# Performance work log

Measured on AMD Instinct MI355X. Metric: run time of the kernel, lower is better.

The kernel has to match this reference:

```python
import math
import jax, jax.numpy as jnp
import numpy as np

D_MODEL = 512
NUM_HEADS = 8
FACTOR = 128
B, T = 16, 768


def setup_inputs() -> dict:
    key = jax.random.key(0)
    ks = jax.random.split(key, 8)
    s_in = 1.0 / math.sqrt(D_MODEL)
    x = jax.random.normal(ks[0], (B, T, D_MODEL), dtype=jnp.float32)
    Wqkv = jax.random.normal(ks[1], (3 * D_MODEL, D_MODEL), dtype=jnp.float32) * s_in
    bqkv = jax.random.normal(ks[2], (3 * D_MODEL,), dtype=jnp.float32) * s_in
    Wconv = jax.random.normal(ks[3], (D_MODEL, D_MODEL, 3), dtype=jnp.float32) * (1.0 / math.sqrt(3 * D_MODEL))
    bconv = jax.random.normal(ks[4], (D_MODEL,), dtype=jnp.float32) * s_in
    gamma = jnp.ones((D_MODEL,), dtype=jnp.float32)
    beta = jnp.zeros((D_MODEL,), dtype=jnp.float32)
    return {"x": x, "Wqkv": Wqkv, "bqkv": bqkv, "Wconv": Wconv, "bconv": bconv, "gamma": gamma, "beta": beta}


def reference(x, Wqkv, bqkv, Wconv, bconv, gamma, beta):
    Bq, Tq, D = x.shape
    H, dk = NUM_HEADS, D // NUM_HEADS
    # --- ProbAttention ---
    qkv = x @ Wqkv.T + bqkv                         # [B,T,3D]
    q, k, v = jnp.split(qkv, 3, axis=-1)
    q = q.reshape(Bq, Tq, H, dk).transpose(0, 2, 1, 3)   # [B,H,T,dk]
    k = k.reshape(Bq, Tq, H, dk).transpose(0, 2, 1, 3)
    v = v.reshape(Bq, Tq, H, dk).transpose(0, 2, 1, 3)
    U = FACTOR * int(math.log(Tq))                  # == T for our config
    scores = jnp.einsum('bhqd,bhkd->bhqk', q, k) / math.sqrt(dk)  # [B,H,T,T]
    top_vals, _ = jax.lax.top_k(scores, U)          # descending-sorted, like torch.topk
    attn = jax.nn.softmax(top_vals, axis=-1)        # [B,H,T,U]
    out = jnp.einsum('bhqu,bhud->bhqd', attn, v)    # requires U == T, as in torch
    attn_out = out.transpose(0, 2, 1, 3).reshape(Bq, Tq, D)
    # --- strided conv branch: Conv1d(D, D, k=3, s=2, p=1) ---
    xc = x.transpose(0, 2, 1)                       # [B,D,T]
    yc = jax.lax.conv_general_dilated(xc, Wconv, window_strides=(2,), padding=[(1, 1)],
                                      dimension_numbers=('NCH', 'OIH', 'NCH'))
    yc = yc + bconv[None, :, None]
    x_conv = yc.transpose(0, 2, 1)                  # [B,T//2,D]
    # --- residual + LayerNorm ---
    res = attn_out[:, ::2, :] + x_conv
    mu = jnp.mean(res, axis=-1, keepdims=True)
    var = jnp.mean(jnp.square(res - mu), axis=-1, keepdims=True)
    y = (res - mu) * jax.lax.rsqrt(var + 1e-5) * gamma + beta
    return y  # dropout is identity in eval mode
```

## Files before the change

kernel.cpp:

```cpp
#include <hip/hip_runtime.h>
#include <hip/hip_bf16.h>
#include <hip/hip_fp16.h>
#include <stdint.h>
#include <math.h>

#define TSEQ 768
#define TOUT 384
#define DM   512
#define NH   8
#define DKH  64

typedef short bf16x8 __attribute__((ext_vector_type(8)));
typedef float f32x4  __attribute__((ext_vector_type(4)));
typedef __fp16 f16x2 __attribute__((ext_vector_type(2)));

__device__ __forceinline__ unsigned short f2bf(float f){
  unsigned int u = __float_as_uint(f);
  unsigned int r = (u + 0x7FFFu + ((u >> 16) & 1u)) >> 16;
  return (unsigned short)r;
}

#define MFMA(a,b,c) __builtin_amdgcn_mfma_f32_16x16x32_bf16((a),(b),(c),0,0,0)

typedef __attribute__((address_space(1))) const void* gas_ptr;
typedef __attribute__((address_space(3))) void*       las_ptr;
__device__ __forceinline__ void gload16(const void* g, void* l){
  __builtin_amdgcn_global_load_lds((gas_ptr)g, (las_ptr)l, 16, 0, 0);
}

__device__ __forceinline__ unsigned xlane_xor_u(unsigned x, int dl){
  int xi = (int)x;
  if (dl == 1)      return (unsigned)__builtin_amdgcn_update_dpp(xi, xi, 0xB1, 0xF, 0xF, true);
  else if (dl == 2) return (unsigned)__builtin_amdgcn_update_dpp(xi, xi, 0x4E, 0xF, 0xF, true);
  else if (dl == 4) return (unsigned)__builtin_amdgcn_ds_swizzle(xi, 0x101F);
  else if (dl == 8) return (unsigned)__builtin_amdgcn_update_dpp(xi, xi, 0x128, 0xF, 0xF, true);
  else return (unsigned)__shfl_xor(xi, dl, 64);
}
__device__ __forceinline__ float xlane_xor_f(float x, int dl){
  return __int_as_float((int)xlane_xor_u((unsigned)__float_as_int(x), dl));
}

__device__ __forceinline__ unsigned pmax2(unsigned a, unsigned b){
  f16x2 r = __builtin_elementwise_max(*reinterpret_cast<f16x2*>(&a),
                                      *reinterpret_cast<f16x2*>(&b));
  return *reinterpret_cast<unsigned*>(&r);
}
__device__ __forceinline__ unsigned pmin2(unsigned a, unsigned b){
  f16x2 r = __builtin_elementwise_min(*reinterpret_cast<f16x2*>(&a),
                                      *reinterpret_cast<f16x2*>(&b));
  return *reinterpret_cast<unsigned*>(&r);
}
__device__ __forceinline__ unsigned pkrtz(float a, float b){
  f16x2 h = __builtin_amdgcn_cvt_pkrtz(a, b);
  return *reinterpret_cast<unsigned*>(&h);
}
__device__ __forceinline__ float lo16f(unsigned u){
  f16x2 h = *reinterpret_cast<f16x2*>(&u); return (float)h[0];
}
__device__ __forceinline__ float hi16f(unsigned u){
  f16x2 h = *reinterpret_cast<f16x2*>(&u); return (float)h[1];
}

__global__ __launch_bounds__(256) void k_cvt(const float* __restrict__ in,
                                             unsigned short* __restrict__ out, int n){
  int i = (blockIdx.x * 256 + threadIdx.x) * 8;
  if (i >= n) return;
  float4 a = *reinterpret_cast<const float4*>(in + i);
  float4 b = *reinterpret_cast<const float4*>(in + i + 4);
  unsigned short u[8] = {f2bf(a.x),f2bf(a.y),f2bf(a.z),f2bf(a.w),
                         f2bf(b.x),f2bf(b.y),f2bf(b.z),f2bf(b.w)};
  *reinterpret_cast<bf16x8*>(out + i) = *reinterpret_cast<bf16x8*>(u);
}

__global__ __launch_bounds__(256) void k_cvt_wconv(const float* __restrict__ w,
                                                   unsigned short* __restrict__ o){
  int idx = blockIdx.x * 256 + threadIdx.x;
  float w0 = w[idx*3+0], w1 = w[idx*3+1], w2 = w[idx*3+2];
  o[idx]          = f2bf(w0);
  o[262144 + idx] = f2bf(w1);
  o[524288 + idx] = f2bf(w2);
}

__global__ __launch_bounds__(256) void k_qkv(const unsigned short* __restrict__ xb,
    const unsigned short* __restrict__ wq, const float* __restrict__ bias,
    unsigned short* __restrict__ qe, unsigned short* __restrict__ kb,
    unsigned short* __restrict__ vb){
  __shared__ unsigned short sA[128*32];
  __shared__ unsigned short sB[128*32];
  int bm = blockIdx.x % 96, bn = blockIdx.x / 96;
  int m0 = bm*128, n0 = bn*128;
  int tid = threadIdx.x, w = tid>>6, l = tid&63;
  int wr = w>>1, wc = w&1, lr = l&15, lk = (l>>4)*8;

  int srow = w*32 + (l>>2);
  int scol = (l&3)*8;
  const unsigned short* gA = xb + (size_t)(m0 + srow)*DM + scol;
  const unsigned short* gB = wq + (size_t)(n0 + srow)*DM + scol;
  unsigned short* dA = sA + w*1024;
  unsigned short* dB = sB + w*1024;

  const unsigned short* ra = sA + (wr*64 + lr)*32 + lk;
  const unsigned short* rb = sB + (wc*64 + lr)*32 + lk;

  f32x4 z = {0.f,0.f,0.f,0.f};
  f32x4 acc[4][4] = {{z,z,z,z},{z,z,z,z},{z,z,z,z},{z,z,z,z}};

  #pragma unroll 1
  for (int ks=0; ks<16; ++ks){
    int k0 = ks*32;
    gload16(gA + k0,          dA);
    gload16(gA + 16*DM + k0,  dA + 512);
    gload16(gB + k0,          dB);
    gload16(gB + 16*DM + k0,  dB + 512);
    __syncthreads();
    bf16x8 af[4], bfr[4];
    #pragma unroll
    for (int f=0; f<4; ++f){
      af[f]  = *reinterpret_cast<const bf16x8*>(ra + f*512);
      bfr[f] = *reinterpret_cast<const bf16x8*>(rb + f*512);
    }
    #pragma unroll
    for (int fq=0; fq<4; ++fq)
      #pragma unroll
      for (int fn=0; fn<4; ++fn)
        acc[fq][fn] = MFMA(af[fq], bfr[fn], acc[fq][fn]);
    __syncthreads();
  }

  int region = n0 >> 9;
  #pragma unroll
  for (int fq=0; fq<4; ++fq)
    #pragma unroll
    for (int fn=0; fn<4; ++fn)
      #pragma unroll
      for (int r=0; r<4; ++r){
        int m = m0 + wr*64 + fq*16 + (l>>4)*4 + r;
        int b = m / TSEQ, t = m - b*TSEQ;
        int n = n0 + wc*64 + fn*16 + lr;
        float val = acc[fq][fn][r] + bias[n];
        unsigned short bv = f2bf(val);
        int bh = b*NH + ((n>>6)&7); int d = n & 63;
        if (region == 0){ if((t&1)==0) qe[((size_t)bh*TOUT + (t>>1))*DKH + d] = bv; }
        else if (region == 1){ kb[((size_t)bh*TSEQ + t)*DKH + d] = bv; }
        else { vb[((size_t)bh*TSEQ + t)*DKH + d] = bv; }
      }
}

__global__ __launch_bounds__(256) void k_vt(const unsigned short* __restrict__ vb,
                                            unsigned short* __restrict__ vT){
  __shared__ unsigned short tile[64][72];
  int bh = blockIdx.x / 12, tt = blockIdx.x % 12;
  int t0 = tt*64;
  int tid = threadIdx.x;
  int r = tid >> 2, c0 = (tid & 3) * 16;
  const unsigned short* src = vb + ((size_t)bh*TSEQ + t0 + r)*DKH + c0;
  *reinterpret_cast<bf16x8*>(&tile[r][c0])   = *reinterpret_cast<const bf16x8*>(src);
  *reinterpret_cast<bf16x8*>(&tile[r][c0+8]) = *reinterpret_cast<const bf16x8*>(src + 8);
  __syncthreads();
  int d = r;
  unsigned short tmp[16];
  #pragma unroll
  for (int j=0;j<16;++j) tmp[j] = tile[c0+j][d];
  unsigned short* dst = vT + ((size_t)bh*DKH + d)*TSEQ + t0 + c0;
  *reinterpret_cast<bf16x8*>(dst)     = *reinterpret_cast<bf16x8*>(tmp);
  *reinterpret_cast<bf16x8*>(dst + 8) = *reinterpret_cast<bf16x8*>(tmp + 8);
}

#define SQ_ROWB 3088
__global__ __launch_bounds__(512, 4) void k_attn(const unsigned short* __restrict__ qe,
    const unsigned short* __restrict__ kb, const unsigned short* __restrict__ vT,
    float* __restrict__ attn){
  __shared__ alignas(16) char sq_raw[16*SQ_ROWB];
  int bh = blockIdx.x / 24, qb = blockIdx.x % 24;
  int tid = threadIdx.x, w = tid>>6, l = tid&63, lr = l&15, lk = (l>>4)*8;

  const unsigned short* qbase = qe + ((size_t)bh*TOUT + qb*16)*DKH;
  bf16x8 qa0 = *reinterpret_cast<const bf16x8*>(qbase + lr*DKH + lk);
  bf16x8 qa1 = *reinterpret_cast<const bf16x8*>(qbase + lr*DKH + 32 + lk);
  const unsigned short* kbase = kb + (size_t)bh*TSEQ*DKH;
  #pragma unroll
  for (int i=0;i<6;++i){
    int nt = w + 8*i;
    const unsigned short* kr = kbase + (size_t)(nt*16 + lr)*DKH + lk;
    bf16x8 B0 = *reinterpret_cast<const bf16x8*>(kr);
    bf16x8 B1 = *reinterpret_cast<const bf16x8*>(kr + 32);
    f32x4 c = {0.f,0.f,0.f,0.f};
    c = MFMA(qa0,B0,c);
    c = MFMA(qa1,B1,c);
    int col = nt*16 + lr;
    int A = col*4;
    int sw = A ^ (((A >> 8) & 7) << 4);
    #pragma unroll
    for (int r=0;r<4;++r){
      int qr = (l>>4)*4 + r;
      *reinterpret_cast<float*>(sq_raw + qr*SQ_ROWB + sw) = c[r] * 0.125f;
    }
  }
  __syncthreads();

  {
    char* rowA = sq_raw + (w*2)*SQ_ROWB;
    char* rowB = rowA + SQ_ROWB;
    unsigned wv[16];
    if (l < 48){
      #pragma unroll
      for (int i4=0;i4<4;++i4){
        int A = l*64 + i4*16;
        int Asw = A ^ (((A >> 8) & 7) << 4);
        f32x4 va = *reinterpret_cast<f32x4*>(rowA + Asw);
        f32x4 vb = *reinterpret_cast<f32x4*>(rowB + Asw);
        wv[i4*4+0] = pkrtz(va[0], vb[0]);
        wv[i4*4+1] = pkrtz(va[1], vb[1]);
        wv[i4*4+2] = pkrtz(va[2], vb[2]);
        wv[i4*4+3] = pkrtz(va[3], vb[3]);
      }
    } else {
      #pragma unroll
      for (int j=0;j<16;++j) wv[j] = 0xFC00FC00u;
    }
    int lane16 = l << 4;
    #pragma unroll
    for (int k = 2; k <= 1024; k <<= 1){
      #pragma unroll
      for (int D = k>>1; D >= 16; D >>= 1){
        int dl = D >> 4;
        bool sel = ((lane16 & k) == 0) == ((l & dl) == 0);
        #pragma unroll
        for (int j=0;j<16;++j){
          unsigned y  = xlane_xor_u(wv[j], dl);
          unsigned mx = pmax2(wv[j], y), mn = pmin2(wv[j], y);
          wv[j] = sel ? mx : mn;
        }
      }
      #pragma unroll
      for (int D = ((k>>1) > 8 ? 8 : (k>>1)); D >= 1; D >>= 1){
        #pragma unroll
        for (int j=0;j<16;++j){
          if ((j & D) == 0){
            int j2 = j | D;
            unsigned mx = pmax2(wv[j], wv[j2]), mn = pmin2(wv[j], wv[j2]);
            if (k <= 8){
              if ((j & k) == 0){ wv[j] = mx; wv[j2] = mn; }
              else             { wv[j] = mn; wv[j2] = mx; }
            } else {
              bool up = (k == 16) ? ((l & 1) == 0) : ((lane16 & k) == 0);
              wv[j]  = up ? mx : mn;
              wv[j2] = up ? mn : mx;
            }
          }
        }
      }
    }
    #pragma unroll 1
    for (int half=0; half<2; ++half){
      float xf[16];
      #pragma unroll
      for (int j=0;j<16;++j) xf[j] = half ? hi16f(wv[j]) : lo16f(wv[j]);
      float mx0 = __shfl(xf[0], 0, 64);
      float s = 0.f;
      #pragma unroll
      for (int j=0;j<16;++j){ xf[j] = __expf(xf[j]-mx0); s += xf[j]; }
      #pragma unroll
      for (int o=1;o<64;o<<=1) s += xlane_xor_f(s, o);
      float inv = 1.f / s;
      if (l < 48){
        unsigned short u[16];
        #pragma unroll
        for (int j=0;j<16;++j) u[j] = f2bf(xf[j]*inv);
        char* pp = (half ? rowB : rowA) + l*32;
        *reinterpret_cast<bf16x8*>(pp)      = *reinterpret_cast<bf16x8*>(u);
        *reinterpret_cast<bf16x8*>(pp + 16) = *reinterpret_cast<bf16x8*>(u + 8);
      }
    }
  }
  __syncthreads();

  if (w < 4){
    f32x4 o = {0.f,0.f,0.f,0.f};
    const unsigned short* vtb = vT + ((size_t)bh*DKH + w*16 + lr)*TSEQ + lk;
    const char* prow = sq_raw + lr*SQ_ROWB + (l>>4)*16;
    #pragma unroll
    for (int ks=0; ks<24; ++ks){
      bf16x8 a  = *reinterpret_cast<const bf16x8*>(prow + ks*64);
      bf16x8 bb = *reinterpret_cast<const bf16x8*>(vtb + ks*32);
      o = MFMA(a,bb,o);
    }
    int b = bh >> 3, h = bh & 7;
    float* ab = attn + ((size_t)b*TOUT + qb*16)*DM + h*DKH + w*16 + lr;
    #pragma unroll
    for (int r=0;r<4;++r){
      int qr = (l>>4)*4 + r;
      ab[(size_t)qr*DM] = o[r];
    }
  }
}

__global__ __launch_bounds__(256) void k_conv(const unsigned short* __restrict__ xb,
    const unsigned short* __restrict__ wc, const float* __restrict__ bconv,
    float* __restrict__ res){
  __shared__ unsigned short sA[128*32];
  __shared__ unsigned short sB[128*32];
  int bm = blockIdx.x % 48, bn = blockIdx.x / 48;
  int m0 = bm*128, n0 = bn*128;
  int tid = threadIdx.x, w = tid>>6, l = tid&63;
  int wr = w>>1, wc2 = w&1, lr = l&15, lk = (l>>4)*8;
  int b = m0 / TOUT, t0 = m0 - b*TOUT;

  int srow = w*32 + (l>>2);
  int scol = (l&3)*8;
  const unsigned short* xrow = xb + (size_t)b*TSEQ*DM;
  unsigned short* dA = sA + w*1024;
  unsigned short* dB = sB + w*1024;
  const unsigned short* ra  = sA + (wr*64 + lr)*32 + lk;
  const unsigned short* rb_ = sB + (wc2*64 + lr)*32 + lk;

  f32x4 z = {0.f,0.f,0.f,0.f};
  f32x4 acc[4][4] = {{z,z,z,z},{z,z,z,z},{z,z,z,z},{z,z,z,z}};
  bool zfix = (t0 == 0);

  #pragma unroll 1
  for (int j=0; j<3; ++j){
    int tin0 = 2*(t0 + srow) + j - 1;
    int tin0c = tin0 < 0 ? 0 : tin0;
    const unsigned short* gA0 = xrow + (size_t)tin0c*DM + scol;
    const unsigned short* gA1 = xrow + (size_t)(tin0 + 32)*DM + scol;
    const unsigned short* gB  = wc + (size_t)j*262144 + (size_t)(n0 + srow)*DM + scol;
    bool dz = zfix && (j == 0);
    #pragma unroll 1
    for (int ks=0; ks<16; ++ks){
      int k0 = ks*32;
      gload16(gA0 + k0,         dA);
      gload16(gA1 + k0,         dA + 512);
      gload16(gB + k0,          dB);
      gload16(gB + 16*DM + k0,  dB + 512);
      __syncthreads();
      if (dz && tid < 4){
        bf16x8 zz = {0,0,0,0,0,0,0,0};
        *reinterpret_cast<bf16x8*>(sA + tid*8) = zz;
      }
      __syncthreads();
      bf16x8 af[4], bfr[4];
      #pragma unroll
      for (int f=0; f<4; ++f){
        af[f]  = *reinterpret_cast<const bf16x8*>(ra  + f*512);
        bfr[f] = *reinterpret_cast<const bf16x8*>(rb_ + f*512);
      }
      #pragma unroll
      for (int fq=0; fq<4; ++fq)
        #pragma unroll
        for (int fn=0; fn<4; ++fn)
          acc[fq][fn] = MFMA(af[fq], bfr[fn], acc[fq][fn]);
      __syncthreads();
    }
  }

  #pragma unroll
  for (int fq=0; fq<4; ++fq)
    #pragma unroll
    for (int fn=0; fn<4; ++fn)
      #pragma unroll
      for (int r=0; r<4; ++r){
        int t = t0 + wr*64 + fq*16 + (l>>4)*4 + r;
        int n = n0 + wc2*64 + fn*16 + lr;
        size_t idx = ((size_t)b*TOUT + t)*DM + n;
        res[idx] = acc[fq][fn][r] + bconv[n] + res[idx];
      }
}

__global__ __launch_bounds__(256) void k_ln(const float* __restrict__ res,
    const float* __restrict__ gamma, const float* __restrict__ beta,
    float* __restrict__ out){
  int row = blockIdx.x*4 + (threadIdx.x>>6);
  int l = threadIdx.x & 63;
  const float* rp = res + (size_t)row*DM + l*8;
  float4 v0 = *reinterpret_cast<const float4*>(rp);
  float4 v1 = *reinterpret_cast<const float4*>(rp + 4);
  float s = v0.x+v0.y+v0.z+v0.w + v1.x+v1.y+v1.z+v1.w;
  #pragma unroll
  for (int o=1;o<64;o<<=1) s += __shfl_xor(s, o, 64);
  float mean = s * (1.f/512.f);
  float d0=v0.x-mean, d1=v0.y-mean, d2=v0.z-mean, d3=v0.w-mean;
  float d4=v1.x-mean, d5=v1.y-mean, d6=v1.z-mean, d7=v1.w-mean;
  float q = d0*d0+d1*d1+d2*d2+d3*d3+d4*d4+d5*d5+d6*d6+d7*d7;
  #pragma unroll
  for (int o=1;o<64;o<<=1) q += __shfl_xor(q, o, 64);
  float var = q * (1.f/512.f);
  float inv = rsqrtf(var + 1e-5f);
  float4 g0 = *reinterpret_cast<const float4*>(gamma + l*8);
  float4 g1 = *reinterpret_cast<const float4*>(gamma + l*8 + 4);
  float4 b0 = *reinterpret_cast<const float4*>(beta + l*8);
  float4 b1 = *reinterpret_cast<const float4*>(beta + l*8 + 4);
  float4 o0, o1;
  o0.x = d0*inv*g0.x + b0.x; o0.y = d1*inv*g0.y + b0.y;
  o0.z = d2*inv*g0.z + b0.z; o0.w = d3*inv*g0.w + b0.w;
  o1.x = d4*inv*g1.x + b1.x; o1.y = d5*inv*g1.y + b1.y;
  o1.z = d6*inv*g1.z + b1.z; o1.w = d7*inv*g1.w + b1.w;
  float* op = out + (size_t)row*DM + l*8;
  *reinterpret_cast<float4*>(op)     = o0;
  *reinterpret_cast<float4*>(op + 4) = o1;
}

extern "C" void kernel_launch(void* const* d_in, const int* in_sizes, int n_in,
                              void* d_out, int out_size, void* d_ws, size_t ws_size,
                              hipStream_t stream){
  const float* x     = (const float*)d_in[0];
  const float* Wqkv  = (const float*)d_in[1];
  const float* bqkv  = (const float*)d_in[2];
  const float* Wconv = (const float*)d_in[3];
  const float* bconv = (const float*)d_in[4];
  const float* gamma = (const float*)d_in[5];
  const float* beta  = (const float*)d_in[6];
  float* out = (float*)d_out;

  char* ws = (char*)d_ws;
  size_t off = 0;
  auto alloc = [&](size_t bytes)->char*{
    char* p = ws + off; off += (bytes + 255) & ~(size_t)255; return p;
  };
  unsigned short* xb  = (unsigned short*)alloc(6291456ull*2);
  unsigned short* wqb = (unsigned short*)alloc(786432ull*2);
  unsigned short* wc3 = (unsigned short*)alloc(786432ull*2);
  unsigned short* qeb = (unsigned short*)alloc(3145728ull*2);
  unsigned short* kbb = (unsigned short*)alloc(6291456ull*2);
  unsigned short* vbb = (unsigned short*)alloc(6291456ull*2);
  unsigned short* vtb = (unsigned short*)alloc(6291456ull*2);
  float*          resb = (float*)alloc(3145728ull*4);

  k_cvt<<<dim3(3072), dim3(256), 0, stream>>>(x, xb, 6291456);
  k_cvt<<<dim3(384),  dim3(256), 0, stream>>>(Wqkv, wqb, 786432);
  k_cvt_wconv<<<dim3(1024), dim3(256), 0, stream>>>(Wconv, wc3);
  k_qkv<<<dim3(1152), dim3(256), 0, stream>>>(xb, wqb, bqkv, qeb, kbb, vbb);
  k_vt<<<dim3(1536), dim3(256), 0, stream>>>(vbb, vtb);
  k_attn<<<dim3(3072), dim3(512), 0, stream>>>(qeb, kbb, vtb, resb);
  k_conv<<<dim3(192), dim3(256), 0, stream>>>(xb, wc3, bconv, resb);
  k_ln<<<dim3(1536), dim3(256), 0, stream>>>(resb, gamma, beta, out);
}
```

Measured before the change: 240.7 us.

## Merge conversion kernels, simplify bitonic sort direction, halve conv N-tile

The three fp32-to-bf16 conversion launches become one kernel that dispatches on block index, removing two launches. The bitonic sort in the attention kernel now flips the sign bit of the packed fp16 values so that every stage sorts in a single direction, which drops the per-lane direction selects. The conv GEMM tile narrows from 128 to 64 output columns, doubling the grid from 192 to 384 blocks to fill more CUs, at the cost of reading more A tiles per output.

```diff
diff --git a/kernel.cpp b/kernel.cpp
--- a/kernel.cpp
+++ b/kernel.cpp
@@ -61,24 +61,33 @@
   f16x2 h = *reinterpret_cast<f16x2*>(&u); return (float)h[1];
 }
 
-__global__ __launch_bounds__(256) void k_cvt(const float* __restrict__ in,
-                                             unsigned short* __restrict__ out, int n){
-  int i = (blockIdx.x * 256 + threadIdx.x) * 8;
-  if (i >= n) return;
-  float4 a = *reinterpret_cast<const float4*>(in + i);
-  float4 b = *reinterpret_cast<const float4*>(in + i + 4);
+__device__ __forceinline__ void cvt8(const float* __restrict__ in,
+                                     unsigned short* __restrict__ out){
+  float4 a = *reinterpret_cast<const float4*>(in);
+  float4 b = *reinterpret_cast<const float4*>(in + 4);
   unsigned short u[8] = {f2bf(a.x),f2bf(a.y),f2bf(a.z),f2bf(a.w),
                          f2bf(b.x),f2bf(b.y),f2bf(b.z),f2bf(b.w)};
-  *reinterpret_cast<bf16x8*>(out + i) = *reinterpret_cast<bf16x8*>(u);
-}
-
-__global__ __launch_bounds__(256) void k_cvt_wconv(const float* __restrict__ w,
-                                                   unsigned short* __restrict__ o){
-  int idx = blockIdx.x * 256 + threadIdx.x;
-  float w0 = w[idx*3+0], w1 = w[idx*3+1], w2 = w[idx*3+2];
-  o[idx]          = f2bf(w0);
-  o[262144 + idx] = f2bf(w1);
-  o[524288 + idx] = f2bf(w2);
+  *reinterpret_cast<bf16x8*>(out) = *reinterpret_cast<bf16x8*>(u);
+}
+
+__global__ __launch_bounds__(256) void k_cvt_all(const float* __restrict__ x,
+    const float* __restrict__ wq, const float* __restrict__ wconv,
+    unsigned short* __restrict__ xb, unsigned short* __restrict__ wqb,
+    unsigned short* __restrict__ wc3){
+  int bid = blockIdx.x;
+  if (bid < 3072){
+    int i = (bid*256 + threadIdx.x)*8;
+    cvt8(x + i, xb + i);
+  } else if (bid < 3456){
+    int i = ((bid-3072)*256 + threadIdx.x)*8;
+    cvt8(wq + i, wqb + i);
+  } else {
+    int idx = (bid-3456)*256 + threadIdx.x;
+    float w0 = wconv[idx*3+0], w1 = wconv[idx*3+1], w2 = wconv[idx*3+2];
+    wc3[idx]          = f2bf(w0);
+    wc3[262144 + idx] = f2bf(w1);
+    wc3[524288 + idx] = f2bf(w2);
+  }
 }
 
 __global__ __launch_bounds__(256) void k_qkv(const unsigned short* __restrict__ xb,
@@ -218,34 +227,47 @@
       #pragma unroll
       for (int j=0;j<16;++j) wv[j] = 0xFC00FC00u;
     }
-    int lane16 = l << 4;
     #pragma unroll
     for (int k = 2; k <= 1024; k <<= 1){
-      #pragma unroll
-      for (int D = k>>1; D >= 16; D >>= 1){
-        int dl = D >> 4;
-        bool sel = ((lane16 & k) == 0) == ((l & dl) == 0);
-        #pragma unroll
-        for (int j=0;j<16;++j){
-          unsigned y  = xlane_xor_u(wv[j], dl);
-          unsigned mx = pmax2(wv[j], y), mn = pmin2(wv[j], y);
-          wv[j] = sel ? mx : mn;
+      if (k >= 16){
+        bool up = (k == 16) ? ((l & 1) == 0) : ((l & (k >> 4)) == 0);
+        unsigned negmask = up ? 0u : 0x80008000u;
+        #pragma unroll
+        for (int j=0;j<16;++j) wv[j] ^= negmask;
+        #pragma unroll
+        for (int D = k>>1; D >= 16; D >>= 1){
+          int dl = D >> 4;
+          bool sel = (l & dl) == 0;
+          #pragma unroll
+          for (int j=0;j<16;++j){
+            unsigned y  = xlane_xor_u(wv[j], dl);
+            unsigned mx = pmax2(wv[j], y), mn = pmin2(wv[j], y);
+            wv[j] = sel ? mx : mn;
+          }
         }
-      }
-      #pragma unroll
-      for (int D = ((k>>1) > 8 ? 8 : (k>>1)); D >= 1; D >>= 1){
-        #pragma unroll
-        for (int j=0;j<16;++j){
-          if ((j & D) == 0){
-            int j2 = j | D;
-            unsigned mx = pmax2(wv[j], wv[j2]), mn = pmin2(wv[j], wv[j2]);
-            if (k <= 8){
+        #pragma unroll
+        for (int D = 8; D >= 1; D >>= 1){
+          #pragma unroll
+          for (int j=0;j<16;++j){
+            if ((j & D) == 0){
+              int j2 = j | D;
+              unsigned mx = pmax2(wv[j], wv[j2]), mn = pmin2(wv[j], wv[j2]);
+              wv[j] = mx; wv[j2] = mn;
+            }
+          }
+        }
+        #pragma unroll
+        for (int j=0;j<16;++j) wv[j] ^= negmask;
+      } else {
+        #pragma unroll
+        for (int D = k>>1; D >= 1; D >>= 1){
+          #pragma unroll
+          for (int j=0;j<16;++j){
+            if ((j & D) == 0){
+              int j2 = j | D;
+              unsigned mx = pmax2(wv[j], wv[j2]), mn = pmin2(wv[j], wv[j2]);
               if ((j & k) == 0){ wv[j] = mx; wv[j2] = mn; }
               else             { wv[j] = mn; wv[j2] = mx; }
-            } else {
-              bool up = (k == 16) ? ((l & 1) == 0) : ((lane16 & k) == 0);
-              wv[j]  = up ? mx : mn;
-              wv[j2] = up ? mn : mx;
             }
           }
         }
@@ -299,56 +321,55 @@
     const unsigned short* __restrict__ wc, const float* __restrict__ bconv,
     float* __restrict__ res){
   __shared__ unsigned short sA[128*32];
-  __shared__ unsigned short sB[128*32];
+  __shared__ unsigned short sB[64*32];
   int bm = blockIdx.x % 48, bn = blockIdx.x / 48;
-  int m0 = bm*128, n0 = bn*128;
+  int m0 = bm*128, n0 = bn*64;
   int tid = threadIdx.x, w = tid>>6, l = tid&63;
   int wr = w>>1, wc2 = w&1, lr = l&15, lk = (l>>4)*8;
   int b = m0 / TOUT, t0 = m0 - b*TOUT;
 
-  int srow = w*32 + (l>>2);
+  int srowA = w*32 + (l>>2);
+  int srowB = w*16 + (l>>2);
   int scol = (l&3)*8;
   const unsigned short* xrow = xb + (size_t)b*TSEQ*DM;
   unsigned short* dA = sA + w*1024;
-  unsigned short* dB = sB + w*1024;
+  unsigned short* dB = sB + w*512;
   const unsigned short* ra  = sA + (wr*64 + lr)*32 + lk;
-  const unsigned short* rb_ = sB + (wc2*64 + lr)*32 + lk;
+  const unsigned short* rb_ = sB + (wc2*32 + lr)*32 + lk;
 
   f32x4 z = {0.f,0.f,0.f,0.f};
-  f32x4 acc[4][4] = {{z,z,z,z},{z,z,z,z},{z,z,z,z},{z,z,z,z}};
+  f32x4 acc[4][2] = {{z,z},{z,z},{z,z},{z,z}};
   bool zfix = (t0 == 0);
 
   #pragma unroll 1
   for (int j=0; j<3; ++j){
-    int tin0 = 2*(t0 + srow) + j - 1;
+    int tin0 = 2*(t0 + srowA) + j - 1;
     int tin0c = tin0 < 0 ? 0 : tin0;
     const unsigned short* gA0 = xrow + (size_t)tin0c*DM + scol;
     const unsigned short* gA1 = xrow + (size_t)(tin0 + 32)*DM + scol;
-    const unsigned short* gB  = wc + (size_t)j*262144 + (size_t)(n0 + srow)*DM + scol;
+    const unsigned short* gB  = wc + (size_t)j*262144 + (size_t)(n0 + srowB)*DM + scol;
     bool dz = zfix && (j == 0);
     #pragma unroll 1
     for (int ks=0; ks<16; ++ks){
       int k0 = ks*32;
-      gload16(gA0 + k0,         dA);
-      gload16(gA1 + k0,         dA + 512);
-      gload16(gB + k0,          dB);
-      gload16(gB + 16*DM + k0,  dB + 512);
+      gload16(gA0 + k0, dA);
+      gload16(gA1 + k0, dA + 512);
+      gload16(gB + k0,  dB);
       __syncthreads();
       if (dz && tid < 4){
         bf16x8 zz = {0,0,0,0,0,0,0,0};
         *reinterpret_cast<bf16x8*>(sA + tid*8) = zz;
       }
       __syncthreads();
-      bf16x8 af[4], bfr[4];
-      #pragma unroll
-      for (int f=0; f<4; ++f){
-        af[f]  = *reinterpret_cast<const bf16x8*>(ra  + f*512);
-        bfr[f] = *reinterpret_cast<const bf16x8*>(rb_ + f*512);
-      }
+      bf16x8 af[4], bfr[2];
+      #pragma unroll
+      for (int f=0; f<4; ++f) af[f] = *reinterpret_cast<const bf16x8*>(ra + f*512);
+      #pragma unroll
+      for (int f=0; f<2; ++f) bfr[f] = *reinterpret_cast<const bf16x8*>(rb_ + f*512);
       #pragma unroll
       for (int fq=0; fq<4; ++fq)
         #pragma unroll
-        for (int fn=0; fn<4; ++fn)
+        for (int fn=0; fn<2; ++fn)
           acc[fq][fn] = MFMA(af[fq], bfr[fn], acc[fq][fn]);
       __syncthreads();
     }
@@ -357,11 +378,11 @@
   #pragma unroll
   for (int fq=0; fq<4; ++fq)
     #pragma unroll
-    for (int fn=0; fn<4; ++fn)
+    for (int fn=0; fn<2; ++fn)
       #pragma unroll
       for (int r=0; r<4; ++r){
         int t = t0 + wr*64 + fq*16 + (l>>4)*4 + r;
-        int n = n0 + wc2*64 + fn*16 + lr;
+        int n = n0 + wc2*32 + fn*16 + lr;
         size_t idx = ((size_t)b*TOUT + t)*DM + n;
         res[idx] = acc[fq][fn][r] + bconv[n] + res[idx];
       }
@@ -426,12 +447,10 @@
   unsigned short* vtb = (unsigned short*)alloc(6291456ull*2);
   float*          resb = (float*)alloc(3145728ull*4);
 
-  k_cvt<<<dim3(3072), dim3(256), 0, stream>>>(x, xb, 6291456);
-  k_cvt<<<dim3(384),  dim3(256), 0, stream>>>(Wqkv, wqb, 786432);
-  k_cvt_wconv<<<dim3(1024), dim3(256), 0, stream>>>(Wconv, wc3);
+  k_cvt_all<<<dim3(4480), dim3(256), 0, stream>>>(x, Wqkv, Wconv, xb, wqb, wc3);
   k_qkv<<<dim3(1152), dim3(256), 0, stream>>>(xb, wqb, bqkv, qeb, kbb, vbb);
   k_vt<<<dim3(1536), dim3(256), 0, stream>>>(vbb, vtb);
   k_attn<<<dim3(3072), dim3(512), 0, stream>>>(qeb, kbb, vtb, resb);
-  k_conv<<<dim3(192), dim3(256), 0, stream>>>(xb, wc3, bconv, resb);
+  k_conv<<<dim3(384), dim3(256), 0, stream>>>(xb, wc3, bconv, resb);
   k_ln<<<dim3(1536), dim3(256), 0, stream>>>(resb, gamma, beta, out);
 }
```

Measured after the change: 368.9 us. 53.3% more time.
